# Performance work log

Measured on AMD Instinct MI355X. Metric: run time of the kernel, lower is better.

The kernel has to match this reference:

```python
import jax, jax.numpy as jnp
import numpy as np

B, N, D, K, S = 16, 1024, 256, 16, 512
TEMP = 0.5   # self.temperature, set externally in the repo
EPS = 1e-10


def _gumbel(key, shape):
    u = jax.random.uniform(key, shape, dtype=jnp.float32)
    return -jnp.log(-jnp.log(u + EPS) + EPS)


def setup_inputs() -> dict:
    key = jax.random.key(0)
    k1, k2, k3 = jax.random.split(key, 3)
    return {
        "ze": jax.random.normal(k1, (B, N, D), dtype=jnp.float32),
        "c_logits": jax.random.normal(k2, (B, K), dtype=jnp.float32),
        "books": jax.random.normal(k3, (K, S, D), dtype=jnp.float32),
        "log_param_q": jnp.asarray(np.log(0.5), dtype=jnp.float32),
        "log_param_q_cls": jnp.asarray(np.log(0.5), dtype=jnp.float32),
        "is_train": 1,
    }


def reference(ze, c_logits, books, log_param_q, log_param_q_cls, is_train):
    # training-path forward of GaussianVectorQuantizer
    param_q = 1.0 + jnp.exp(log_param_q)
    precision_q = 0.5 / jnp.clip(param_q, 1e-10)
    param_q_cls = 1.0 + jnp.exp(log_param_q_cls)
    precision_q_cls = 0.5 / jnp.clip(param_q_cls, 1e-10)

    gkey = jax.random.key(42)
    kg1, kg2 = jax.random.split(gkey)

    # gumbel-softmax over clusters: (B, K)
    c_probs = jax.nn.softmax(
        (c_logits * precision_q_cls + _gumbel(kg1, c_logits.shape)) / TEMP, axis=-1
    )

    # pairwise squared distances to every codebook entry of every cluster: (B, N, K, S)
    z2 = jnp.sum(ze * ze, axis=-1)[:, :, None, None]          # (B, N, 1, 1)
    b2 = jnp.sum(books * books, axis=-1)[None, None]          # (1, 1, K, S)
    cross = jnp.einsum('bnd,ksd->bnks', ze, books)            # (B, N, K, S)
    logit_all = -(z2 - 2.0 * cross + b2) * precision_q        # (B, N, K, S)

    # cluster-probability-weighted logits: (B, N, S)
    logits = jnp.einsum('bnks,bk->bns', logit_all, c_probs)

    # gumbel-softmax encodings per cluster, then weighted codebook matmul
    enc = jax.nn.softmax((logit_all + _gumbel(kg2, logit_all.shape)) / TEMP, axis=-1)
    zq = jnp.einsum('bnks,ksd,bk->bnd', enc, books, c_probs)  # (B, N, D)

    prob = jax.nn.softmax(logits, axis=-1)
    log_prob = jax.nn.log_softmax(logits, axis=-1)
    return zq, precision_q, prob, log_prob
```

## Files before the change

### kernel.cpp

```cpp
#include <hip/hip_runtime.h>
#include <cstdint>
#include <cstddef>

#define JAX_PARTITIONABLE 1

namespace {

constexpr int Bsz = 16, Nn = 1024, Dd = 256, Kk = 16, Ss = 512;
constexpr uint32_t BN = (uint32_t)Bsz * Nn;
constexpr int ZQ_SIZE = Bsz * Nn * Dd;
constexpr int PQ_OFF = ZQ_SIZE;
constexpr int PROB_OFF = ZQ_SIZE + 1;
constexpr int BNS = Bsz * Nn * Ss;
constexpr int LP_OFF = PROB_OFF + BNS;

constexpr int WS_CP = 0;
constexpr int WS_B2 = 256;
constexpr int WS_WB2 = WS_B2 + Kk * Ss;
constexpr int WS_WBOOKS = WS_WB2 + Bsz * Ss;
constexpr int WS_BBF = WS_WBOOKS + Bsz * Ss * Dd;
constexpr int WS_BTF = WS_BBF + (Kk * Ss * Dd) / 2;

typedef __attribute__((ext_vector_type(8))) short bf16x8;
typedef __attribute__((ext_vector_type(4))) short short4v;
typedef __attribute__((ext_vector_type(4))) float f32x4;

struct KP { uint32_t a, b; };

__host__ __device__ constexpr KP tf2x32(uint32_t k0, uint32_t k1,
                                        uint32_t x0, uint32_t x1) {
  uint32_t ks[3] = {k0, k1, k0 ^ k1 ^ 0x1BD11BDAu};
  const int rot[2][4] = {{13, 15, 26, 6}, {17, 29, 16, 24}};
  x0 += ks[0];
  x1 += ks[1];
#pragma unroll
  for (int i = 0; i < 5; ++i) {
#pragma unroll
    for (int j = 0; j < 4; ++j) {
      int r = rot[i & 1][j];
      x0 += x1;
      x1 = (x1 << r) | (x1 >> (32 - r));
      x1 ^= x0;
    }
    x0 += ks[(i + 1) % 3];
    x1 += ks[(i + 2) % 3] + (uint32_t)(i + 1);
  }
  return {x0, x1};
}

#if JAX_PARTITIONABLE
constexpr KP KG1 = tf2x32(0u, 42u, 0u, 0u);
constexpr KP KG2 = tf2x32(0u, 42u, 0u, 1u);
#else
constexpr KP KH0 = tf2x32(0u, 42u, 0u, 2u);
constexpr KP KH1 = tf2x32(0u, 42u, 1u, 3u);
constexpr KP KG1 = {KH0.a, KH1.a};
constexpr KP KG2 = {KH0.b, KH1.b};
#endif

__device__ __forceinline__ float jax_gumbel(KP key, uint32_t idx, uint32_t half) {
#if JAX_PARTITIONABLE
  (void)half;
  KP h = tf2x32(key.a, key.b, 0u, idx);
  uint32_t bits = h.a ^ h.b;
#else
  uint32_t lo = idx < half ? idx : idx - half;
  KP h = tf2x32(key.a, key.b, lo, lo + half);
  uint32_t bits = idx < half ? h.a : h.b;
#endif
  float u = __uint_as_float((bits >> 9) | 0x3F800000u) - 1.0f;
  return -__logf(-__logf(u + 1e-10f) + 1e-10f);
}

__device__ __forceinline__ float prec_q(const float* p) {
  return 0.5f / fmaxf(1.0f + expf(p[0]), 1e-10f);
}

__device__ __forceinline__ short f2bf(float x) {
  uint32_t u = __float_as_uint(x);
  uint32_t r = (u + 0x7FFFu + ((u >> 16) & 1u)) >> 16;
  return (short)r;
}

__global__ void __launch_bounds__(256) cprobs_kernel(
    const float* __restrict__ c_logits, const float* __restrict__ lpq,
    const float* __restrict__ lpq_cls, float* __restrict__ ws,
    float* __restrict__ out) {
  __shared__ float sl[256];
  const int t = threadIdx.x;
  const float pqc = prec_q(lpq_cls);
  float g = jax_gumbel(KG1, (uint32_t)t, 128u);
  sl[t] = (c_logits[t] * pqc + g) * 2.0f;
  __syncthreads();
  const int b = t >> 4;
  float m = -3.0e38f;
  for (int j = 0; j < 16; ++j) m = fmaxf(m, sl[b * 16 + j]);
  float sum = 0.f;
  for (int j = 0; j < 16; ++j) sum += expf(sl[b * 16 + j] - m);
  ws[WS_CP + t] = expf(sl[t] - m) / sum;
  if (t == 0) out[PQ_OFF] = prec_q(lpq);
}

__global__ void __launch_bounds__(256) norms_kernel(
    const float* __restrict__ books, float* __restrict__ ws) {
  const int row = blockIdx.x * 4 + (threadIdx.x >> 6);
  const int lane = threadIdx.x & 63;
  float4 v = ((const float4*)(books + (size_t)row * Dd))[lane];
  float s = v.x * v.x + v.y * v.y + v.z * v.z + v.w * v.w;
#pragma unroll
  for (int d = 1; d < 64; d <<= 1) s += __shfl_xor(s, d);
  if (lane == 0) ws[WS_B2 + row] = s;
}

__global__ void __launch_bounds__(256) prep_kernel(
    const float* __restrict__ books, float* __restrict__ ws) {
  __shared__ short tile[16 * 256];
  const int k = blockIdx.x >> 5;
  const int s0 = (blockIdx.x & 31) << 4;
  short* bbf = (short*)(ws + WS_BBF);
  short* btf = (short*)(ws + WS_BTF);
  const int t = threadIdx.x;
#pragma unroll
  for (int i = 0; i < 4; ++i) {
    int idx = t + 256 * i;
    int r = idx >> 6, dq = idx & 63;
    float4 v = ((const float4*)books)[(size_t)(k * Ss + s0 + r) * 64 + dq];
    short4v h = {f2bf(v.x), f2bf(v.y), f2bf(v.z), f2bf(v.w)};
    *(short4v*)&bbf[(size_t)(k * Ss + s0 + r) * 256 + dq * 4] = h;
    *(short4v*)&tile[r * 256 + dq * 4] = h;
  }
  __syncthreads();
  const int d = t;
  short vals[16];
#pragma unroll
  for (int r = 0; r < 16; ++r) vals[r] = tile[r * 256 + d];
  bf16x8 lo, hi;
#pragma unroll
  for (int r = 0; r < 8; ++r) { lo[r] = vals[r]; hi[r] = vals[r + 8]; }
  size_t base = ((size_t)(k * 256 + d)) * 512 + s0;
  *(bf16x8*)&btf[base] = lo;
  *(bf16x8*)&btf[base + 8] = hi;
}

__global__ void __launch_bounds__(256) wbooks_kernel(
    const float* __restrict__ books, float* __restrict__ ws) {
  const int bs = blockIdx.x;
  const int b = bs >> 9, s = bs & 511;
  const int d = threadIdx.x;
  const float* cp = ws + WS_CP + b * 16;
  float acc = 0.f;
#pragma unroll
  for (int k = 0; k < 16; ++k)
    acc = fmaf(cp[k], books[((size_t)(k * Ss + s)) * Dd + d], acc);
  ws[WS_WBOOKS + ((size_t)(b * Ss + s)) * Dd + d] = acc;
  if (d == 0) {
    float a2 = 0.f;
#pragma unroll
    for (int k = 0; k < 16; ++k) a2 = fmaf(cp[k], ws[WS_B2 + k * Ss + s], a2);
    ws[WS_WB2 + b * Ss + s] = a2;
  }
}

__global__ void __launch_bounds__(256, 4) logits_kernel(
    const float* __restrict__ ze, const float* __restrict__ lpq,
    const float* __restrict__ ws, float* __restrict__ out) {
  __shared__ float ze_s[8 * 256];
  __shared__ float ls[8 * 512];
  const int b = blockIdx.x >> 7;
  const int n0 = (blockIdx.x & 127) << 3;
  const int t = threadIdx.x;
  const float pq = prec_q(lpq);

  {
    const float4* zin = (const float4*)(ze + (size_t)(b * Nn + n0) * Dd);
    float4* zo = (float4*)ze_s;
    zo[t] = zin[t];
    zo[t + 256] = zin[t + 256];
  }
  __syncthreads();

  float acc0[8], acc1[8];
#pragma unroll
  for (int r = 0; r < 8; ++r) { acc0[r] = 0.f; acc1[r] = 0.f; }
  const int s0 = t, s1 = t + 256;
  const float4* w4_0 = (const float4*)(ws + WS_WBOOKS + (size_t)(b * Ss + s0) * Dd);
  const float4* w4_1 = (const float4*)(ws + WS_WBOOKS + (size_t)(b * Ss + s1) * Dd);
  const float4* z4 = (const float4*)ze_s;
  for (int dq = 0; dq < 64; ++dq) {
    float4 u0 = w4_0[dq], u1 = w4_1[dq];
#pragma unroll
    for (int r = 0; r < 8; ++r) {
      float4 z = z4[r * 64 + dq];
      acc0[r] = fmaf(z.x, u0.x, fmaf(z.y, u0.y, fmaf(z.z, u0.z, fmaf(z.w, u0.w, acc0[r]))));
      acc1[r] = fmaf(z.x, u1.x, fmaf(z.y, u1.y, fmaf(z.z, u1.z, fmaf(z.w, u1.w, acc1[r]))));
    }
  }
  const float wb2v0 = ws[WS_WB2 + b * Ss + s0];
  const float wb2v1 = ws[WS_WB2 + b * Ss + s1];
#pragma unroll
  for (int r = 0; r < 8; ++r) {
    ls[r * 512 + s0] = pq * (2.f * acc0[r] - wb2v0);
    ls[r * 512 + s1] = pq * (2.f * acc1[r] - wb2v1);
  }
  __syncthreads();

  const int r = t >> 5, c = t & 31;
  float m = -3.0e38f;
#pragma unroll
  for (int j = 0; j < 16; ++j) m = fmaxf(m, ls[r * 512 + c + 32 * j]);
#pragma unroll
  for (int d = 1; d < 32; d <<= 1) m = fmaxf(m, __shfl_xor(m, d));
  float ev[16];
  float sum = 0.f;
#pragma unroll
  for (int j = 0; j < 16; ++j) {
    ev[j] = expf(ls[r * 512 + c + 32 * j] - m);
    sum += ev[j];
  }
#pragma unroll
  for (int d = 1; d < 32; d <<= 1) sum += __shfl_xor(sum, d);
  const float inv = 1.f / sum;
  const float lsum = logf(sum);
  const size_t obase = (size_t)(b * Nn + n0 + r) * Ss;
  float* pr = out + PROB_OFF + obase;
  float* lp = out + LP_OFF + obase;
#pragma unroll
  for (int j = 0; j < 16; ++j) {
    int s = c + 32 * j;
    pr[s] = ev[j] * inv;
    lp[s] = (ls[r * 512 + s] - m) - lsum;
  }
}

__global__ void __launch_bounds__(512, 4) zq_kernel(
    const float* __restrict__ ze, const float* __restrict__ lpq,
    const float* __restrict__ ws, float* __restrict__ out) {
  __shared__ short ze_s[32 * 264];
  __shared__ short enc_s[32 * 520];
  __shared__ float2 redms[32][8];
  __shared__ float cpk[16];

  const int b = blockIdx.x >> 5;
  const int n0 = (blockIdx.x & 31) << 5;
  const int t = threadIdx.x;
  const int w = t >> 6, lane = t & 63, c = lane & 15, q = lane >> 4;
  const float pq = prec_q(lpq);
  const short* bbf = (const short*)(ws + WS_BBF);
  const short* btf = (const short*)(ws + WS_BTF);
  const float* b2p = ws + WS_B2;

  if (t < 16) cpk[t] = ws[WS_CP + b * 16 + t];
#pragma unroll
  for (int i = 0; i < 4; ++i) {
    int idx = t + 512 * i;
    int r = idx >> 6, dq = idx & 63;
    float4 v = ((const float4*)ze)[(size_t)(b * Nn + n0 + r) * 64 + dq];
    short4v h = {f2bf(v.x), f2bf(v.y), f2bf(v.z), f2bf(v.w)};
    *(short4v*)&ze_s[r * 264 + dq * 4] = h;
  }
  __syncthreads();

  f32x4 acc2[2][2];
#pragma unroll
  for (int rt = 0; rt < 2; ++rt)
#pragma unroll
    for (int dt = 0; dt < 2; ++dt) acc2[rt][dt] = (f32x4)(0.f);

  for (int k = 0; k < 16; ++k) {
    f32x4 acc1[2][4];
#pragma unroll
    for (int rt = 0; rt < 2; ++rt)
#pragma unroll
      for (int st = 0; st < 4; ++st) acc1[rt][st] = (f32x4)(0.f);
    for (int dstep = 0; dstep < 8; ++dstep) {
      bf16x8 a0 = *(const bf16x8*)&ze_s[(c) * 264 + dstep * 32 + q * 8];
      bf16x8 a1 = *(const bf16x8*)&ze_s[(16 + c) * 264 + dstep * 32 + q * 8];
#pragma unroll
      for (int st = 0; st < 4; ++st) {
        bf16x8 bB = *(const bf16x8*)&bbf[((size_t)(k * Ss + w * 64 + st * 16 + c)) * 256 +
                                         dstep * 32 + q * 8];
        acc1[0][st] = __builtin_amdgcn_mfma_f32_16x16x32_bf16(a0, bB, acc1[0][st], 0, 0, 0);
        acc1[1][st] = __builtin_amdgcn_mfma_f32_16x16x32_bf16(a1, bB, acc1[1][st], 0, 0, 0);
      }
    }

    float b2v[4];
#pragma unroll
    for (int st = 0; st < 4; ++st) b2v[st] = b2p[k * Ss + w * 64 + st * 16 + c];
    float mx[2][4], sm[2][4];
#pragma unroll
    for (int rt = 0; rt < 2; ++rt)
#pragma unroll
      for (int reg = 0; reg < 4; ++reg) mx[rt][reg] = -3.0e38f;
#pragma unroll
    for (int rt = 0; rt < 2; ++rt)
#pragma unroll
      for (int st = 0; st < 4; ++st)
#pragma unroll
        for (int reg = 0; reg < 4; ++reg) {
          int row = n0 + rt * 16 + q * 4 + reg;
          uint32_t gi = ((uint32_t)(b * Nn + row) * (uint32_t)Kk + (uint32_t)k) * (uint32_t)Ss +
                        (uint32_t)(w * 64 + st * 16 + c);
          float g = jax_gumbel(KG2, gi, 0u);
          float v = ((2.f * acc1[rt][st][reg] - b2v[st]) * pq + g) * 2.f;
          acc1[rt][st][reg] = v;
          mx[rt][reg] = fmaxf(mx[rt][reg], v);
        }
#pragma unroll
    for (int m = 1; m < 16; m <<= 1)
#pragma unroll
      for (int rt = 0; rt < 2; ++rt)
#pragma unroll
        for (int reg = 0; reg < 4; ++reg)
          mx[rt][reg] = fmaxf(mx[rt][reg], __shfl_xor(mx[rt][reg], m));
#pragma unroll
    for (int rt = 0; rt < 2; ++rt)
#pragma unroll
      for (int reg = 0; reg < 4; ++reg) sm[rt][reg] = 0.f;
#pragma unroll
    for (int rt = 0; rt < 2; ++rt)
#pragma unroll
      for (int st = 0; st < 4; ++st)
#pragma unroll
        for (int reg = 0; reg < 4; ++reg) {
          float e = __expf(acc1[rt][st][reg] - mx[rt][reg]);
          acc1[rt][st][reg] = e;
          sm[rt][reg] += e;
        }
#pragma unroll
    for (int m = 1; m < 16; m <<= 1)
#pragma unroll
      for (int rt = 0; rt < 2; ++rt)
#pragma unroll
        for (int reg = 0; reg < 4; ++reg) sm[rt][reg] += __shfl_xor(sm[rt][reg], m);
    if (c == 0) {
#pragma unroll
      for (int rt = 0; rt < 2; ++rt)
#pragma unroll
        for (int reg = 0; reg < 4; ++reg) {
          int rl = rt * 16 + q * 4 + reg;
          redms[rl][w] = make_float2(mx[rt][reg], sm[rt][reg]);
        }
    }
    __syncthreads();

    const float cpv = cpk[k];
#pragma unroll
    for (int rt = 0; rt < 2; ++rt)
#pragma unroll
      for (int reg = 0; reg < 4; ++reg) {
        int rl = rt * 16 + q * 4 + reg;
        float M = mx[rt][reg];
#pragma unroll
        for (int w2 = 0; w2 < 8; ++w2) M = fmaxf(M, redms[rl][w2].x);
        float T = 0.f;
#pragma unroll
        for (int w2 = 0; w2 < 8; ++w2)
          T = fmaf(redms[rl][w2].y, __expf(redms[rl][w2].x - M), T);
        float scale = cpv * __expf(mx[rt][reg] - M) * __builtin_amdgcn_rcpf(T);
#pragma unroll
        for (int st = 0; st < 4; ++st)
          enc_s[rl * 520 + w * 64 + st * 16 + c] = f2bf(acc1[rt][st][reg] * scale);
      }
    __syncthreads();

    for (int ss = 0; ss < 16; ++ss) {
      bf16x8 a0 = *(const bf16x8*)&enc_s[(c) * 520 + ss * 32 + q * 8];
      bf16x8 a1 = *(const bf16x8*)&enc_s[(16 + c) * 520 + ss * 32 + q * 8];
#pragma unroll
      for (int dt = 0; dt < 2; ++dt) {
        bf16x8 bB = *(const bf16x8*)&btf[((size_t)(k * 256 + w * 32 + dt * 16 + c)) * 512 +
                                         ss * 32 + q * 8];
        acc2[0][dt] = __builtin_amdgcn_mfma_f32_16x16x32_bf16(a0, bB, acc2[0][dt], 0, 0, 0);
        acc2[1][dt] = __builtin_amdgcn_mfma_f32_16x16x32_bf16(a1, bB, acc2[1][dt], 0, 0, 0);
      }
    }
  }

#pragma unroll
  for (int rt = 0; rt < 2; ++rt)
#pragma unroll
    for (int dt = 0; dt < 2; ++dt)
#pragma unroll
      for (int reg = 0; reg < 4; ++reg) {
        int row = n0 + rt * 16 + q * 4 + reg;
        int d = w * 32 + dt * 16 + c;
        out[(size_t)(b * Nn + row) * Dd + d] = acc2[rt][dt][reg];
      }
}

}

extern "C" void kernel_launch(void* const* d_in, const int* in_sizes, int n_in,
                              void* d_out, int out_size, void* d_ws, size_t ws_size,
                              hipStream_t stream) {
  (void)in_sizes; (void)n_in; (void)out_size; (void)ws_size;
  const float* ze = (const float*)d_in[0];
  const float* c_logits = (const float*)d_in[1];
  const float* books = (const float*)d_in[2];
  const float* lpq = (const float*)d_in[3];
  const float* lpq_cls = (const float*)d_in[4];
  float* out = (float*)d_out;
  float* ws = (float*)d_ws;

  hipLaunchKernelGGL(cprobs_kernel, dim3(1), dim3(256), 0, stream,
                     c_logits, lpq, lpq_cls, ws, out);
  hipLaunchKernelGGL(norms_kernel, dim3(Kk * Ss / 4), dim3(256), 0, stream, books, ws);
  hipLaunchKernelGGL(prep_kernel, dim3(Kk * 32), dim3(256), 0, stream, books, ws);
  hipLaunchKernelGGL(wbooks_kernel, dim3(Bsz * Ss), dim3(256), 0, stream, books, ws);
  hipLaunchKernelGGL(logits_kernel, dim3(Bsz * (Nn / 8)), dim3(256), 0, stream,
                     ze, lpq, ws, out);
  hipLaunchKernelGGL(zq_kernel, dim3(Bsz * (Nn / 32)), dim3(512), 0, stream,
                     ze, lpq, ws, out);
}
```

Measured before the change: 835.6 us.

## Split fused zq kernel into staged GEMM, Gumbel-softmax, GEMM passes over workspace

Replaces the single fused zq kernel with a loop over cluster groups. Each group runs three kernels: a bf16 MFMA GEMM that writes scaled distance logits to a workspace scratch buffer, a row-wise Gumbel-softmax kernel that overwrites the scratch in place with bf16 probabilities weighted by cluster probability, and a second MFMA GEMM that accumulates zq into the output. The group size is picked from the available workspace size, and the code falls back to the fused kernel when the workspace is too small. The goal is to relieve the fused kernel's register and LDS pressure and give each stage its own parallelism, at the cost of large extra global memory traffic (about 32 MB of scratch per cluster) and more kernel launches.

```diff
diff --git a/kernel.cpp b/kernel.cpp
--- a/kernel.cpp
+++ b/kernel.cpp
@@ -20,6 +20,7 @@
 constexpr int WS_WBOOKS = WS_WB2 + Bsz * Ss;
 constexpr int WS_BBF = WS_WBOOKS + Bsz * Ss * Dd;
 constexpr int WS_BTF = WS_BBF + (Kk * Ss * Dd) / 2;
+constexpr int WS_SC = WS_BTF + (Kk * Dd * Ss) / 2;
 
 typedef __attribute__((ext_vector_type(8))) short bf16x8;
 typedef __attribute__((ext_vector_type(4))) short short4v;
@@ -232,12 +233,159 @@
   }
 }
 
+__global__ void __launch_bounds__(512, 4) gemm1s_kernel(
+    const float* __restrict__ ze, const float* __restrict__ lpq,
+    float* __restrict__ ws, int k0, int KG) {
+  __shared__ short ze_s[32 * 264];
+  const int b = blockIdx.x >> 5;
+  const int n0 = (blockIdx.x & 31) << 5;
+  const int t = threadIdx.x;
+  const int w = t >> 6, lane = t & 63, c = lane & 15, q = lane >> 4;
+  const float pq = prec_q(lpq);
+  const short* bbf = (const short*)(ws + WS_BBF);
+  const float* b2p = ws + WS_B2;
+  float* sc = ws + WS_SC;
+
+#pragma unroll
+  for (int i = 0; i < 4; ++i) {
+    int idx = t + 512 * i;
+    int r = idx >> 6, dq = idx & 63;
+    float4 v = ((const float4*)ze)[(size_t)(b * Nn + n0 + r) * 64 + dq];
+    short4v h = {f2bf(v.x), f2bf(v.y), f2bf(v.z), f2bf(v.w)};
+    *(short4v*)&ze_s[r * 264 + dq * 4] = h;
+  }
+  __syncthreads();
+
+  for (int kk = 0; kk < KG; ++kk) {
+    const int k = k0 + kk;
+    f32x4 acc1[2][4];
+#pragma unroll
+    for (int rt = 0; rt < 2; ++rt)
+#pragma unroll
+      for (int st = 0; st < 4; ++st) acc1[rt][st] = (f32x4)(0.f);
+    for (int dstep = 0; dstep < 8; ++dstep) {
+      bf16x8 a0 = *(const bf16x8*)&ze_s[(c) * 264 + dstep * 32 + q * 8];
+      bf16x8 a1 = *(const bf16x8*)&ze_s[(16 + c) * 264 + dstep * 32 + q * 8];
+#pragma unroll
+      for (int st = 0; st < 4; ++st) {
+        bf16x8 bB = *(const bf16x8*)&bbf[((size_t)(k * Ss + w * 64 + st * 16 + c)) * 256 +
+                                         dstep * 32 + q * 8];
+        acc1[0][st] = __builtin_amdgcn_mfma_f32_16x16x32_bf16(a0, bB, acc1[0][st], 0, 0, 0);
+        acc1[1][st] = __builtin_amdgcn_mfma_f32_16x16x32_bf16(a1, bB, acc1[1][st], 0, 0, 0);
+      }
+    }
+    float b2v[4];
+#pragma unroll
+    for (int st = 0; st < 4; ++st) b2v[st] = b2p[k * Ss + w * 64 + st * 16 + c];
+#pragma unroll
+    for (int rt = 0; rt < 2; ++rt)
+#pragma unroll
+      for (int st = 0; st < 4; ++st)
+#pragma unroll
+        for (int reg = 0; reg < 4; ++reg) {
+          int row = n0 + rt * 16 + q * 4 + reg;
+          sc[((size_t)(b * Nn + row) * KG + kk) * Ss + (w * 64 + st * 16 + c)] =
+              (2.f * acc1[rt][st][reg] - b2v[st]) * pq;
+        }
+  }
+}
+
+__global__ void __launch_bounds__(256, 8) gumbel_kernel(
+    float* __restrict__ ws, int k0, int kgshift) {
+  const int t = threadIdx.x;
+  const int row = blockIdx.x * 4 + (t >> 6);
+  const int lane = t & 63;
+  const int bn = row >> kgshift;
+  const int kk = row & ((1 << kgshift) - 1);
+  const int k = k0 + kk;
+  const int b = bn >> 10;
+  const float cpv = ws[WS_CP + b * 16 + k];
+
+  float* sp = ws + WS_SC + (size_t)row * Ss;
+  f32x4 v0 = *(const f32x4*)(sp + lane * 4);
+  f32x4 v1 = *(const f32x4*)(sp + 256 + lane * 4);
+
+  const uint32_t gbase = ((uint32_t)bn * (uint32_t)Kk + (uint32_t)k) * (uint32_t)Ss;
+  float v[8];
+#pragma unroll
+  for (int j = 0; j < 4; ++j) {
+    v[j] = (v0[j] + jax_gumbel(KG2, gbase + (uint32_t)(lane * 4 + j), 0u)) * 2.f;
+    v[4 + j] = (v1[j] + jax_gumbel(KG2, gbase + (uint32_t)(256 + lane * 4 + j), 0u)) * 2.f;
+  }
+  float M = v[0];
+#pragma unroll
+  for (int j = 1; j < 8; ++j) M = fmaxf(M, v[j]);
+#pragma unroll
+  for (int d = 1; d < 64; d <<= 1) M = fmaxf(M, __shfl_xor(M, d));
+  float T = 0.f;
+#pragma unroll
+  for (int j = 0; j < 8; ++j) {
+    v[j] = __expf(v[j] - M);
+    T += v[j];
+  }
+#pragma unroll
+  for (int d = 1; d < 64; d <<= 1) T += __shfl_xor(T, d);
+  const float scale = cpv * __builtin_amdgcn_rcpf(T);
+
+  short* ep = (short*)sp;
+  short4v e0 = {f2bf(v[0] * scale), f2bf(v[1] * scale), f2bf(v[2] * scale), f2bf(v[3] * scale)};
+  short4v e1 = {f2bf(v[4] * scale), f2bf(v[5] * scale), f2bf(v[6] * scale), f2bf(v[7] * scale)};
+  *(short4v*)(ep + lane * 4) = e0;
+  *(short4v*)(ep + 256 + lane * 4) = e1;
+}
+
+__global__ void __launch_bounds__(512, 4) gemm2s_kernel(
+    const float* __restrict__ ws, float* __restrict__ out, int k0, int KG) {
+  const int b = blockIdx.x >> 5;
+  const int n0 = (blockIdx.x & 31) << 5;
+  const int t = threadIdx.x;
+  const int w = t >> 6, lane = t & 63, c = lane & 15, q = lane >> 4;
+  const short* btf = (const short*)(ws + WS_BTF);
+  const short* ep = (const short*)(ws + WS_SC);
+
+  f32x4 acc2[2][2];
+#pragma unroll
+  for (int rt = 0; rt < 2; ++rt)
+#pragma unroll
+    for (int dt = 0; dt < 2; ++dt) acc2[rt][dt] = (f32x4)(0.f);
+
+  for (int kk = 0; kk < KG; ++kk) {
+    const int k = k0 + kk;
+    const size_t ar0 = ((size_t)(b * Nn + n0 + c) * KG + kk) * 1024;
+    const size_t ar1 = ((size_t)(b * Nn + n0 + 16 + c) * KG + kk) * 1024;
+    for (int ss = 0; ss < 16; ++ss) {
+      bf16x8 a0 = *(const bf16x8*)&ep[ar0 + ss * 32 + q * 8];
+      bf16x8 a1 = *(const bf16x8*)&ep[ar1 + ss * 32 + q * 8];
+#pragma unroll
+      for (int dt = 0; dt < 2; ++dt) {
+        bf16x8 bB = *(const bf16x8*)&btf[((size_t)(k * 256 + w * 32 + dt * 16 + c)) * 512 +
+                                         ss * 32 + q * 8];
+        acc2[0][dt] = __builtin_amdgcn_mfma_f32_16x16x32_bf16(a0, bB, acc2[0][dt], 0, 0, 0);
+        acc2[1][dt] = __builtin_amdgcn_mfma_f32_16x16x32_bf16(a1, bB, acc2[1][dt], 0, 0, 0);
+      }
+    }
+  }
+
+#pragma unroll
+  for (int rt = 0; rt < 2; ++rt)
+#pragma unroll
+    for (int dt = 0; dt < 2; ++dt)
+#pragma unroll
+      for (int reg = 0; reg < 4; ++reg) {
+        int row = n0 + rt * 16 + q * 4 + reg;
+        int d = w * 32 + dt * 16 + c;
+        size_t o = (size_t)(b * Nn + row) * Dd + d;
+        if (k0 == 0) out[o] = acc2[rt][dt][reg];
+        else out[o] += acc2[rt][dt][reg];
+      }
+}
+
 __global__ void __launch_bounds__(512, 4) zq_kernel(
     const float* __restrict__ ze, const float* __restrict__ lpq,
     const float* __restrict__ ws, float* __restrict__ out) {
   __shared__ short ze_s[32 * 264];
   __shared__ short enc_s[32 * 520];
-  __shared__ float2 redms[32][8];
+  __shared__ float2 redms[32][9];
   __shared__ float cpk[16];
 
   const int b = blockIdx.x >> 5;
@@ -394,7 +542,7 @@
 extern "C" void kernel_launch(void* const* d_in, const int* in_sizes, int n_in,
                               void* d_out, int out_size, void* d_ws, size_t ws_size,
                               hipStream_t stream) {
-  (void)in_sizes; (void)n_in; (void)out_size; (void)ws_size;
+  (void)in_sizes; (void)n_in; (void)out_size;
   const float* ze = (const float*)d_in[0];
   const float* c_logits = (const float*)d_in[1];
   const float* books = (const float*)d_in[2];
@@ -410,6 +558,28 @@
   hipLaunchKernelGGL(wbooks_kernel, dim3(Bsz * Ss), dim3(256), 0, stream, books, ws);
   hipLaunchKernelGGL(logits_kernel, dim3(Bsz * (Nn / 8)), dim3(256), 0, stream,
                      ze, lpq, ws, out);
-  hipLaunchKernelGGL(zq_kernel, dim3(Bsz * (Nn / 32)), dim3(512), 0, stream,
-                     ze, lpq, ws, out);
-}
+
+  int KG = 0, kgshift = 0;
+  const size_t base_bytes = (size_t)WS_SC * 4;
+  const int cands[3] = {4, 2, 1};
+  const int shifts[3] = {2, 1, 0};
+  for (int i = 0; i < 3; ++i) {
+    size_t need = base_bytes + (size_t)BN * cands[i] * Ss * 4;
+    if (ws_size >= need) { KG = cands[i]; kgshift = shifts[i]; break; }
+  }
+
+  if (KG > 0) {
+    const int rows_per_group = (int)BN * KG;
+    for (int k0 = 0; k0 < Kk; k0 += KG) {
+      hipLaunchKernelGGL(gemm1s_kernel, dim3(Bsz * (Nn / 32)), dim3(512), 0, stream,
+                         ze, lpq, ws, k0, KG);
+      hipLaunchKernelGGL(gumbel_kernel, dim3(rows_per_group / 4), dim3(256), 0, stream,
+                         ws, k0, kgshift);
+      hipLaunchKernelGGL(gemm2s_kernel, dim3(Bsz * (Nn / 32)), dim3(512), 0, stream,
+                         ws, out, k0, KG);
+    }
+  } else {
+    hipLaunchKernelGGL(zq_kernel, dim3(Bsz * (Nn / 32)), dim3(512), 0, stream,
+                       ze, lpq, ws, out);
+  }
+}
```

Measured after the change: 1.473 ms. +76.3%, slower.

## Compute weighted logits with bf16 MFMA and register-resident softmax

Applied to the files above, without the earlier changes.

The weighted codebook is now stored in bf16, and the fp32 FMA logits kernel is replaced by an MFMA 16x16x32 bf16 GEMM over 32-row tiles. The softmax and log-softmax are computed straight from the accumulator registers, using cross-lane shuffles and a cross-wave max/sum reduction in shared memory, so no full logits tile is staged in LDS. This cuts ALU time and halves the read traffic for the weighted books. In exchange, logits go through bf16 inputs, which lowers precision of prob and log_prob.

```diff
diff --git a/kernel.cpp b/kernel.cpp
--- a/kernel.cpp
+++ b/kernel.cpp
@@ -17,8 +17,8 @@
 constexpr int WS_CP = 0;
 constexpr int WS_B2 = 256;
 constexpr int WS_WB2 = WS_B2 + Kk * Ss;
-constexpr int WS_WBOOKS = WS_WB2 + Bsz * Ss;
-constexpr int WS_BBF = WS_WBOOKS + Bsz * Ss * Dd;
+constexpr int WS_WBF = WS_WB2 + Bsz * Ss;
+constexpr int WS_BBF = WS_WBF + Bsz * Ss * Dd;
 constexpr int WS_BTF = WS_BBF + (Kk * Ss * Dd) / 2;
 
 typedef __attribute__((ext_vector_type(8))) short bf16x8;
@@ -152,7 +152,8 @@
 #pragma unroll
   for (int k = 0; k < 16; ++k)
     acc = fmaf(cp[k], books[((size_t)(k * Ss + s)) * Dd + d], acc);
-  ws[WS_WBOOKS + ((size_t)(b * Ss + s)) * Dd + d] = acc;
+  short* wbf = (short*)(ws + WS_WBF);
+  wbf[((size_t)(b * Ss + s)) * Dd + d] = f2bf(acc);
   if (d == 0) {
     float a2 = 0.f;
 #pragma unroll
@@ -161,75 +162,119 @@
   }
 }
 
-__global__ void __launch_bounds__(256, 4) logits_kernel(
+__global__ void __launch_bounds__(512, 4) mlogits_kernel(
     const float* __restrict__ ze, const float* __restrict__ lpq,
     const float* __restrict__ ws, float* __restrict__ out) {
-  __shared__ float ze_s[8 * 256];
-  __shared__ float ls[8 * 512];
-  const int b = blockIdx.x >> 7;
-  const int n0 = (blockIdx.x & 127) << 3;
+  __shared__ short ze_s[32 * 264];
+  __shared__ float2 redms[32][9];
+  const int b = blockIdx.x >> 5;
+  const int n0 = (blockIdx.x & 31) << 5;
   const int t = threadIdx.x;
+  const int w = t >> 6, lane = t & 63, c = lane & 15, q = lane >> 4;
   const float pq = prec_q(lpq);
-
-  {
-    const float4* zin = (const float4*)(ze + (size_t)(b * Nn + n0) * Dd);
-    float4* zo = (float4*)ze_s;
-    zo[t] = zin[t];
-    zo[t + 256] = zin[t + 256];
+  const short* wbf = (const short*)(ws + WS_WBF);
+  const float* wb2 = ws + WS_WB2;
+
+#pragma unroll
+  for (int i = 0; i < 4; ++i) {
+    int idx = t + 512 * i;
+    int r = idx >> 6, dq = idx & 63;
+    float4 v = ((const float4*)ze)[(size_t)(b * Nn + n0 + r) * 64 + dq];
+    short4v h = {f2bf(v.x), f2bf(v.y), f2bf(v.z), f2bf(v.w)};
+    *(short4v*)&ze_s[r * 264 + dq * 4] = h;
   }
   __syncthreads();
 
-  float acc0[8], acc1[8];
-#pragma unroll
-  for (int r = 0; r < 8; ++r) { acc0[r] = 0.f; acc1[r] = 0.f; }
-  const int s0 = t, s1 = t + 256;
-  const float4* w4_0 = (const float4*)(ws + WS_WBOOKS + (size_t)(b * Ss + s0) * Dd);
-  const float4* w4_1 = (const float4*)(ws + WS_WBOOKS + (size_t)(b * Ss + s1) * Dd);
-  const float4* z4 = (const float4*)ze_s;
-  for (int dq = 0; dq < 64; ++dq) {
-    float4 u0 = w4_0[dq], u1 = w4_1[dq];
-#pragma unroll
-    for (int r = 0; r < 8; ++r) {
-      float4 z = z4[r * 64 + dq];
-      acc0[r] = fmaf(z.x, u0.x, fmaf(z.y, u0.y, fmaf(z.z, u0.z, fmaf(z.w, u0.w, acc0[r]))));
-      acc1[r] = fmaf(z.x, u1.x, fmaf(z.y, u1.y, fmaf(z.z, u1.z, fmaf(z.w, u1.w, acc1[r]))));
-    }
-  }
-  const float wb2v0 = ws[WS_WB2 + b * Ss + s0];
-  const float wb2v1 = ws[WS_WB2 + b * Ss + s1];
-#pragma unroll
-  for (int r = 0; r < 8; ++r) {
-    ls[r * 512 + s0] = pq * (2.f * acc0[r] - wb2v0);
-    ls[r * 512 + s1] = pq * (2.f * acc1[r] - wb2v1);
+  f32x4 acc1[2][4];
+#pragma unroll
+  for (int rt = 0; rt < 2; ++rt)
+#pragma unroll
+    for (int st = 0; st < 4; ++st) acc1[rt][st] = (f32x4)(0.f);
+  for (int dstep = 0; dstep < 8; ++dstep) {
+    bf16x8 a0 = *(const bf16x8*)&ze_s[(c) * 264 + dstep * 32 + q * 8];
+    bf16x8 a1 = *(const bf16x8*)&ze_s[(16 + c) * 264 + dstep * 32 + q * 8];
+#pragma unroll
+    for (int st = 0; st < 4; ++st) {
+      bf16x8 bB = *(const bf16x8*)&wbf[((size_t)(b * Ss + w * 64 + st * 16 + c)) * 256 +
+                                       dstep * 32 + q * 8];
+      acc1[0][st] = __builtin_amdgcn_mfma_f32_16x16x32_bf16(a0, bB, acc1[0][st], 0, 0, 0);
+      acc1[1][st] = __builtin_amdgcn_mfma_f32_16x16x32_bf16(a1, bB, acc1[1][st], 0, 0, 0);
+    }
+  }
+
+  float mx[2][4], sm[2][4];
+#pragma unroll
+  for (int rt = 0; rt < 2; ++rt)
+#pragma unroll
+    for (int reg = 0; reg < 4; ++reg) mx[rt][reg] = -3.0e38f;
+#pragma unroll
+  for (int st = 0; st < 4; ++st) {
+    const float wb2v = wb2[b * Ss + w * 64 + st * 16 + c];
+#pragma unroll
+    for (int rt = 0; rt < 2; ++rt)
+#pragma unroll
+      for (int reg = 0; reg < 4; ++reg) {
+        float v = (2.f * acc1[rt][st][reg] - wb2v) * pq;
+        acc1[rt][st][reg] = v;
+        mx[rt][reg] = fmaxf(mx[rt][reg], v);
+      }
+  }
+#pragma unroll
+  for (int m = 1; m < 16; m <<= 1)
+#pragma unroll
+    for (int rt = 0; rt < 2; ++rt)
+#pragma unroll
+      for (int reg = 0; reg < 4; ++reg)
+        mx[rt][reg] = fmaxf(mx[rt][reg], __shfl_xor(mx[rt][reg], m));
+#pragma unroll
+  for (int rt = 0; rt < 2; ++rt)
+#pragma unroll
+    for (int reg = 0; reg < 4; ++reg) sm[rt][reg] = 0.f;
+#pragma unroll
+  for (int st = 0; st < 4; ++st)
+#pragma unroll
+    for (int rt = 0; rt < 2; ++rt)
+#pragma unroll
+      for (int reg = 0; reg < 4; ++reg)
+        sm[rt][reg] += __expf(acc1[rt][st][reg] - mx[rt][reg]);
+#pragma unroll
+  for (int m = 1; m < 16; m <<= 1)
+#pragma unroll
+    for (int rt = 0; rt < 2; ++rt)
+#pragma unroll
+      for (int reg = 0; reg < 4; ++reg) sm[rt][reg] += __shfl_xor(sm[rt][reg], m);
+  if (c == 0) {
+#pragma unroll
+    for (int rt = 0; rt < 2; ++rt)
+#pragma unroll
+      for (int reg = 0; reg < 4; ++reg)
+        redms[rt * 16 + q * 4 + reg][w] = make_float2(mx[rt][reg], sm[rt][reg]);
   }
   __syncthreads();
 
-  const int r = t >> 5, c = t & 31;
-  float m = -3.0e38f;
-#pragma unroll
-  for (int j = 0; j < 16; ++j) m = fmaxf(m, ls[r * 512 + c + 32 * j]);
-#pragma unroll
-  for (int d = 1; d < 32; d <<= 1) m = fmaxf(m, __shfl_xor(m, d));
-  float ev[16];
-  float sum = 0.f;
-#pragma unroll
-  for (int j = 0; j < 16; ++j) {
-    ev[j] = expf(ls[r * 512 + c + 32 * j] - m);
-    sum += ev[j];
-  }
-#pragma unroll
-  for (int d = 1; d < 32; d <<= 1) sum += __shfl_xor(sum, d);
-  const float inv = 1.f / sum;
-  const float lsum = logf(sum);
-  const size_t obase = (size_t)(b * Nn + n0 + r) * Ss;
-  float* pr = out + PROB_OFF + obase;
-  float* lp = out + LP_OFF + obase;
-#pragma unroll
-  for (int j = 0; j < 16; ++j) {
-    int s = c + 32 * j;
-    pr[s] = ev[j] * inv;
-    lp[s] = (ls[r * 512 + s] - m) - lsum;
-  }
+#pragma unroll
+  for (int rt = 0; rt < 2; ++rt)
+#pragma unroll
+    for (int reg = 0; reg < 4; ++reg) {
+      int rl = rt * 16 + q * 4 + reg;
+      float M = mx[rt][reg];
+#pragma unroll
+      for (int w2 = 0; w2 < 8; ++w2) M = fmaxf(M, redms[rl][w2].x);
+      float T = 0.f;
+#pragma unroll
+      for (int w2 = 0; w2 < 8; ++w2)
+        T = fmaf(redms[rl][w2].y, __expf(redms[rl][w2].x - M), T);
+      const float invT = __builtin_amdgcn_rcpf(T);
+      const float lT = __logf(T);
+      const size_t base = (size_t)(b * Nn + n0 + rl) * Ss;
+#pragma unroll
+      for (int st = 0; st < 4; ++st) {
+        int s = w * 64 + st * 16 + c;
+        float v = acc1[rt][st][reg] - M;
+        out[PROB_OFF + base + s] = __expf(v) * invT;
+        out[LP_OFF + base + s] = v - lT;
+      }
+    }
 }
 
 __global__ void __launch_bounds__(512, 4) zq_kernel(
@@ -237,7 +282,7 @@
     const float* __restrict__ ws, float* __restrict__ out) {
   __shared__ short ze_s[32 * 264];
   __shared__ short enc_s[32 * 520];
-  __shared__ float2 redms[32][8];
+  __shared__ float2 redms[32][9];
   __shared__ float cpk[16];
 
   const int b = blockIdx.x >> 5;
@@ -408,7 +453,7 @@
   hipLaunchKernelGGL(norms_kernel, dim3(Kk * Ss / 4), dim3(256), 0, stream, books, ws);
   hipLaunchKernelGGL(prep_kernel, dim3(Kk * 32), dim3(256), 0, stream, books, ws);
   hipLaunchKernelGGL(wbooks_kernel, dim3(Bsz * Ss), dim3(256), 0, stream, books, ws);
-  hipLaunchKernelGGL(logits_kernel, dim3(Bsz * (Nn / 8)), dim3(256), 0, stream,
+  hipLaunchKernelGGL(mlogits_kernel, dim3(Bsz * (Nn / 32)), dim3(512), 0, stream,
                      ze, lpq, ws, out);
   hipLaunchKernelGGL(zq_kernel, dim3(Bsz * (Nn / 32)), dim3(512), 0, stream,
                      ze, lpq, ws, out);
```

Result: faster. 724.2 us (-13.3%).
